# Kernel optimization log

Hardware: AMD Instinct MI355X
Metric: run time of the kernel (lower is better)

## Reference

```python
import jax, jax.numpy as jnp
import numpy as np


def setup_inputs() -> dict:
    key = jax.random.key(0)
    ks = jax.random.split(key, 4)
    B, T, D, U = 64, 2048, 256, 256
    x = jax.random.normal(ks[0], (B, T, D), dtype=jnp.float32)
    s = 1.0 / np.sqrt(D)
    kz = jax.random.normal(ks[1], (D, U), dtype=jnp.float32) * s
    kr = jax.random.normal(ks[2], (D, U), dtype=jnp.float32) * s
    kh = jax.random.normal(ks[3], (D, U), dtype=jnp.float32) * s
    return {
        'x': x, 'kz': kz, 'kr': kr, 'kh': kh,
        'mz': jnp.ones((U,), jnp.float32), 'mr': jnp.ones((U,), jnp.float32),
        'bz': jnp.zeros((U,), jnp.float32), 'br': jnp.zeros((U,), jnp.float32),
        'bh': jnp.zeros((U,), jnp.float32),
    }


def reference(x, kz, kr, kh, mz, mr, bz, br, bh):
    # Precompute the three input projections for all timesteps (batched GEMMs),
    # then scan the purely elementwise recurrence over time.
    xz = jnp.einsum('btd,du->btu', x, kz) + bz  # [B,T,U]
    xr = jnp.einsum('btd,du->btu', x, kr) + br
    xh = jnp.einsum('btd,du->btu', x, kh) + bh
    B, T, U = xz.shape
    h0 = jnp.zeros((B, U), x.dtype)

    def step(h, inp):
        xz_t, xr_t, xh_t = inp
        r = jnp.tanh(xr_t + h * mr) + 1.0
        z = jax.nn.sigmoid(xz_t + h * mz)
        hh = jnp.tanh(xh_t + r * h)
        out = (1.0 - z) * hh + z * h
        return out, out

    # scan over time axis: move T to leading axis
    xs = (jnp.swapaxes(xz, 0, 1), jnp.swapaxes(xr, 0, 1), jnp.swapaxes(xh, 0, 1))
    _, ys = jax.lax.scan(step, h0, xs)
    return jnp.swapaxes(ys, 0, 1)  # [B,T,U]
```

## Files before the change

kernel.cpp:

```cpp
#include <hip/hip_runtime.h>
#include <hip/hip_bf16.h>

#define BB 64
#define TT 2048
#define DD 256
#define UU 256
#define MM (BB*TT)
#define NN (3*UU)
#define PLANE ((size_t)BB*TT*UU)

typedef _Float16 half8 __attribute__((ext_vector_type(8)));
typedef _Float16 half4 __attribute__((ext_vector_type(4)));
typedef float floatx4 __attribute__((ext_vector_type(4)));

__device__ inline float fexp2(float x){
#if __has_builtin(__builtin_amdgcn_exp2f)
  return __builtin_amdgcn_exp2f(x);
#else
  return exp2f(x);
#endif
}
__device__ inline float frcp(float x){
#if __has_builtin(__builtin_amdgcn_rcpf)
  return __builtin_amdgcn_rcpf(x);
#else
  return 1.0f/x;
#endif
}
__device__ inline float ftanh(float a){
  const float TWO_L2E = 2.8853900817779268f;
  return 1.0f - 2.0f*frcp(fexp2(TWO_L2E*a) + 1.0f);
}
__device__ inline float fsigmoid(float a){
  const float L2E = 1.4426950408889634f;
  return frcp(1.0f + fexp2(-L2E*a));
}

__global__ __launch_bounds__(256) void prep_kernel(const float* __restrict__ kz,
                                                   const float* __restrict__ kr,
                                                   const float* __restrict__ kh,
                                                   _Float16* __restrict__ K16T){
  int o = blockIdx.x*256 + threadIdx.x;
  int n = o >> 8;
  int k = o & 255;
  int p = n >> 8;
  int u = n & 255;
  const float* w = (p==0) ? kz : ((p==1) ? kr : kh);
  K16T[o] = (_Float16)w[k*UU + u];
}

__global__ __launch_bounds__(256) void xcvt_kernel(const float* __restrict__ X,
                                                   _Float16* __restrict__ X16){
  const size_t t = (size_t)blockIdx.x*256 + threadIdx.x;
  #pragma unroll
  for (int i = 0; i < 8; i++){
    const size_t u = ((size_t)i << 20) + t;
    floatx4 v = *(const floatx4*)(X + u*4);
    half4 hv;
    #pragma unroll
    for (int q = 0; q < 4; q++) hv[q] = (_Float16)v[q];
    *(half4*)(X16 + u*4) = hv;
  }
}

#define BM 128
#define BN 128
#define BK 32

__global__ __launch_bounds__(256) void gemm_kernel(const _Float16* __restrict__ X16,
                                                   const _Float16* __restrict__ K16T,
                                                   const float* __restrict__ bz,
                                                   const float* __restrict__ br,
                                                   const float* __restrict__ bh,
                                                   _Float16* __restrict__ P){
  __shared__ __align__(16) _Float16 As[BM*BK];
  __shared__ __align__(16) _Float16 Bs[BN*BK];
  const int tid = threadIdx.x;

  const int l   = blockIdx.y*6 + blockIdx.x;
  const int xcd = l & 7;
  const int idx = l >> 3;
  const int pnl = idx / 6;
  const int by  = xcd*128 + pnl;
  const int bx  = idx - pnl*6;
  const int rowBase = by*BM;
  const int nBase   = bx*BN;

  const int wave = tid >> 6, lane = tid & 63;
  const int wm = wave & 1, wn = wave >> 1;
  const int lrow = lane & 15, lkq = lane >> 4;

  floatx4 acc[4][4] = {};

  const _Float16* aSrc0 = X16 + (size_t)(rowBase + (tid >> 2))*DD + (tid & 3)*8;
  const _Float16* aSrc1 = aSrc0 + (size_t)64*DD;
  const _Float16* bSrc0 = K16T + (size_t)(nBase + (tid >> 2))*DD + (tid & 3)*8;
  const _Float16* bSrc1 = bSrc0 + (size_t)64*DD;

  for (int k0 = 0; k0 < DD; k0 += BK) {
    __syncthreads();
    __builtin_amdgcn_global_load_lds(
        (const __attribute__((address_space(1))) void*)(aSrc0 + k0),
        (__attribute__((address_space(3))) void*)(As + tid*8), 16, 0, 0);
    __builtin_amdgcn_global_load_lds(
        (const __attribute__((address_space(1))) void*)(aSrc1 + k0),
        (__attribute__((address_space(3))) void*)(As + 2048 + tid*8), 16, 0, 0);
    __builtin_amdgcn_global_load_lds(
        (const __attribute__((address_space(1))) void*)(bSrc0 + k0),
        (__attribute__((address_space(3))) void*)(Bs + tid*8), 16, 0, 0);
    __builtin_amdgcn_global_load_lds(
        (const __attribute__((address_space(1))) void*)(bSrc1 + k0),
        (__attribute__((address_space(3))) void*)(Bs + 2048 + tid*8), 16, 0, 0);
    __syncthreads();
    half8 af[4], bf[4];
    #pragma unroll
    for (int i = 0; i < 4; i++)
      af[i] = *(const half8*)&As[(wm*64 + i*16 + lrow)*BK + lkq*8];
    #pragma unroll
    for (int j = 0; j < 4; j++)
      bf[j] = *(const half8*)&Bs[(wn*64 + j*16 + lrow)*BK + lkq*8];
    #pragma unroll
    for (int i = 0; i < 4; i++)
      #pragma unroll
      for (int j = 0; j < 4; j++)
        acc[i][j] = __builtin_amdgcn_mfma_f32_16x16x32_f16(af[i], bf[j], acc[i][j], 0, 0, 0);
  }

  const int p = bx >> 1;
  const int ub = (bx & 1) * 128;
  const float* bias = (p==0) ? bz : ((p==1) ? br : bh);
  _Float16* Pp = P + (size_t)p * PLANE;
  const int bidx = rowBase >> 11;
  const int t0 = (rowBase & 2047) + wm*64 + lkq*4;
  #pragma unroll
  for (int j = 0; j < 4; j++){
    int col = ub + wn*64 + j*16 + lrow;
    float bv = bias[col];
    _Float16* rowp = Pp + (size_t)(bidx*UU + col)*TT + t0;
    #pragma unroll
    for (int i = 0; i < 4; i++){
      half4 v;
      #pragma unroll
      for (int r = 0; r < 4; r++)
        v[r] = (_Float16)(acc[i][j][r] + bv);
      *(half4*)(rowp + i*16) = v;
    }
  }
}

#define PF 16
#define NBUF 4
__global__ __launch_bounds__(64) void scan_kernel(const _Float16* __restrict__ P,
                                                  const float* __restrict__ mz,
                                                  const float* __restrict__ mr,
                                                  float* __restrict__ out){
  const int ci = blockIdx.x*64 + threadIdx.x;
  const int b = ci >> 8;
  const int u = ci & 255;
  const half8* pz = (const half8*)(P + (size_t)ci*TT);
  const half8* pr = (const half8*)(P + PLANE + (size_t)ci*TT);
  const half8* ph = (const half8*)(P + 2*PLANE + (size_t)ci*TT);
  float* po = out + (size_t)b*(TT*UU) + u;
  const float vmz = mz[u], vmr = mr[u];
  float h = 0.0f;

  half8 qz[NBUF][2], qr[NBUF][2], qh[NBUF][2];

#define LOADC(buf, c) do { \
    qz[buf][0] = pz[(c)*2];   qz[buf][1] = pz[(c)*2+1]; \
    qr[buf][0] = pr[(c)*2];   qr[buf][1] = pr[(c)*2+1]; \
    qh[buf][0] = ph[(c)*2];   qh[buf][1] = ph[(c)*2+1]; \
  } while(0)

#define PROC(buf, c) do { \
    _Pragma("unroll") \
    for (int i = 0; i < PF; i++){ \
      float xz = (float)qz[buf][i>>3][i&7]; \
      float xr = (float)qr[buf][i>>3][i&7]; \
      float xh = (float)qh[buf][i>>3][i&7]; \
      float r  = ftanh(xr + h*vmr) + 1.0f; \
      float z  = fsigmoid(xz + h*vmz); \
      float hh = ftanh(xh + r*h); \
      h = (1.0f - z)*hh + z*h; \
      po[(size_t)((c)*PF + i)*UU] = h; \
    } \
    if ((c) + NBUF < NC) LOADC(buf, (c) + NBUF); \
  } while(0)

  const int NC = TT/PF;
  LOADC(0, 0); LOADC(1, 1); LOADC(2, 2); LOADC(3, 3);
  for (int c = 0; c < NC; c += NBUF){
    PROC(0, c);
    PROC(1, c+1);
    PROC(2, c+2);
    PROC(3, c+3);
  }
#undef LOADC
#undef PROC
}

extern "C" void kernel_launch(void* const* d_in, const int* in_sizes, int n_in,
                              void* d_out, int out_size, void* d_ws, size_t ws_size,
                              hipStream_t stream) {
  (void)in_sizes; (void)n_in; (void)out_size; (void)ws_size;
  const float* x  = (const float*)d_in[0];
  const float* kz = (const float*)d_in[1];
  const float* kr = (const float*)d_in[2];
  const float* kh = (const float*)d_in[3];
  const float* mz = (const float*)d_in[4];
  const float* mr = (const float*)d_in[5];
  const float* bz = (const float*)d_in[6];
  const float* br = (const float*)d_in[7];
  const float* bh = (const float*)d_in[8];
  float* out = (float*)d_out;

  _Float16* K16T = (_Float16*)d_ws;
  _Float16* P    = (_Float16*)((char*)d_ws + 393216);
  _Float16* X16  = (_Float16*)d_out;

  hipLaunchKernelGGL(xcvt_kernel, dim3(4096), dim3(256), 0, stream, x, X16);
  hipLaunchKernelGGL(prep_kernel, dim3(NN*DD/256), dim3(256), 0, stream, kz, kr, kh, K16T);
  hipLaunchKernelGGL(gemm_kernel, dim3(NN/BN, MM/BM), dim3(256), 0, stream,
                     X16, K16T, bz, br, bh, P);
  hipLaunchKernelGGL(scan_kernel, dim3(256), dim3(64), 0, stream, P, mz, mr, out);
}
```

Measured before the change: 474.3 us.

## Double-buffer GEMM LDS, fold activation scales into projections, interleave two scan chains

The GEMM now double-buffers its LDS tiles so the next K slice loads while the current one feeds the MFMAs, with one barrier per step instead of two. The exp2 scale factors of sigmoid and tanh are folded into the projection outputs in the GEMM epilogue and into the recurrence weights, so the scan does fewer multiplies per step. The scan gives each thread two independent hidden units, halving the grid to 128 blocks, so two dependent chains can hide each other's latency. The costs are fewer scan waves across the GPU, scaled fp16 values stored in P that may lose some precision, and a single barrier that may not be enough to order async LDS loads against reads of the other buffer.

Result: slower. 561.0 us (+18.3%).

```diff
diff --git a/kernel.cpp b/kernel.cpp
--- a/kernel.cpp
+++ b/kernel.cpp
@@ -26,14 +26,6 @@
 #else
   return 1.0f/x;
 #endif
-}
-__device__ inline float ftanh(float a){
-  const float TWO_L2E = 2.8853900817779268f;
-  return 1.0f - 2.0f*frcp(fexp2(TWO_L2E*a) + 1.0f);
-}
-__device__ inline float fsigmoid(float a){
-  const float L2E = 1.4426950408889634f;
-  return frcp(1.0f + fexp2(-L2E*a));
 }
 
 __global__ __launch_bounds__(256) void prep_kernel(const float* __restrict__ kz,
@@ -66,15 +58,14 @@
 #define BM 128
 #define BN 128
 #define BK 32
-
 __global__ __launch_bounds__(256) void gemm_kernel(const _Float16* __restrict__ X16,
                                                    const _Float16* __restrict__ K16T,
                                                    const float* __restrict__ bz,
                                                    const float* __restrict__ br,
                                                    const float* __restrict__ bh,
                                                    _Float16* __restrict__ P){
-  __shared__ __align__(16) _Float16 As[BM*BK];
-  __shared__ __align__(16) _Float16 Bs[BN*BK];
+  __shared__ __align__(16) _Float16 As[2][BM*BK];
+  __shared__ __align__(16) _Float16 Bs[2][BN*BK];
   const int tid = threadIdx.x;
 
   const int l   = blockIdx.y*6 + blockIdx.x;
@@ -97,38 +88,48 @@
   const _Float16* bSrc0 = K16T + (size_t)(nBase + (tid >> 2))*DD + (tid & 3)*8;
   const _Float16* bSrc1 = bSrc0 + (size_t)64*DD;
 
-  for (int k0 = 0; k0 < DD; k0 += BK) {
-    __syncthreads();
-    __builtin_amdgcn_global_load_lds(
-        (const __attribute__((address_space(1))) void*)(aSrc0 + k0),
-        (__attribute__((address_space(3))) void*)(As + tid*8), 16, 0, 0);
-    __builtin_amdgcn_global_load_lds(
-        (const __attribute__((address_space(1))) void*)(aSrc1 + k0),
-        (__attribute__((address_space(3))) void*)(As + 2048 + tid*8), 16, 0, 0);
-    __builtin_amdgcn_global_load_lds(
-        (const __attribute__((address_space(1))) void*)(bSrc0 + k0),
-        (__attribute__((address_space(3))) void*)(Bs + tid*8), 16, 0, 0);
-    __builtin_amdgcn_global_load_lds(
-        (const __attribute__((address_space(1))) void*)(bSrc1 + k0),
-        (__attribute__((address_space(3))) void*)(Bs + 2048 + tid*8), 16, 0, 0);
-    __syncthreads();
+#define STAGE(buf, k0) do { \
+    __builtin_amdgcn_global_load_lds( \
+        (const __attribute__((address_space(1))) void*)(aSrc0 + (k0)), \
+        (__attribute__((address_space(3))) void*)(&As[(buf)][tid*8]), 16, 0, 0); \
+    __builtin_amdgcn_global_load_lds( \
+        (const __attribute__((address_space(1))) void*)(aSrc1 + (k0)), \
+        (__attribute__((address_space(3))) void*)(&As[(buf)][2048 + tid*8]), 16, 0, 0); \
+    __builtin_amdgcn_global_load_lds( \
+        (const __attribute__((address_space(1))) void*)(bSrc0 + (k0)), \
+        (__attribute__((address_space(3))) void*)(&Bs[(buf)][tid*8]), 16, 0, 0); \
+    __builtin_amdgcn_global_load_lds( \
+        (const __attribute__((address_space(1))) void*)(bSrc1 + (k0)), \
+        (__attribute__((address_space(3))) void*)(&Bs[(buf)][2048 + tid*8]), 16, 0, 0); \
+  } while(0)
+
+  STAGE(0, 0);
+  __syncthreads();
+
+  #pragma unroll
+  for (int kk = 0; kk < 8; kk++){
+    const int cur = kk & 1;
+    if (kk < 7) STAGE(cur ^ 1, (kk + 1)*BK);
     half8 af[4], bf[4];
     #pragma unroll
     for (int i = 0; i < 4; i++)
-      af[i] = *(const half8*)&As[(wm*64 + i*16 + lrow)*BK + lkq*8];
+      af[i] = *(const half8*)&As[cur][(wm*64 + i*16 + lrow)*BK + lkq*8];
     #pragma unroll
     for (int j = 0; j < 4; j++)
-      bf[j] = *(const half8*)&Bs[(wn*64 + j*16 + lrow)*BK + lkq*8];
+      bf[j] = *(const half8*)&Bs[cur][(wn*64 + j*16 + lrow)*BK + lkq*8];
     #pragma unroll
     for (int i = 0; i < 4; i++)
       #pragma unroll
       for (int j = 0; j < 4; j++)
         acc[i][j] = __builtin_amdgcn_mfma_f32_16x16x32_f16(af[i], bf[j], acc[i][j], 0, 0, 0);
-  }
+    __syncthreads();
+  }
+#undef STAGE
 
   const int p = bx >> 1;
   const int ub = (bx & 1) * 128;
   const float* bias = (p==0) ? bz : ((p==1) ? br : bh);
+  const float pscale = (p==0) ? -1.4426950408889634f : 2.8853900817779268f;
   _Float16* Pp = P + (size_t)p * PLANE;
   const int bidx = rowBase >> 11;
   const int t0 = (rowBase & 2047) + wm*64 + lkq*4;
@@ -142,47 +143,69 @@
       half4 v;
       #pragma unroll
       for (int r = 0; r < 4; r++)
-        v[r] = (_Float16)(acc[i][j][r] + bv);
+        v[r] = (_Float16)((acc[i][j][r] + bv) * pscale);
       *(half4*)(rowp + i*16) = v;
     }
   }
 }
 
-#define PF 16
+#define PF 8
 #define NBUF 4
-__global__ __launch_bounds__(64) void scan_kernel(const _Float16* __restrict__ P,
-                                                  const float* __restrict__ mz,
-                                                  const float* __restrict__ mr,
-                                                  float* __restrict__ out){
-  const int ci = blockIdx.x*64 + threadIdx.x;
-  const int b = ci >> 8;
-  const int u = ci & 255;
-  const half8* pz = (const half8*)(P + (size_t)ci*TT);
-  const half8* pr = (const half8*)(P + PLANE + (size_t)ci*TT);
-  const half8* ph = (const half8*)(P + 2*PLANE + (size_t)ci*TT);
-  float* po = out + (size_t)b*(TT*UU) + u;
-  const float vmz = mz[u], vmr = mr[u];
-  float h = 0.0f;
+__global__ __launch_bounds__(64, 1) void scan_kernel(const _Float16* __restrict__ P,
+                                                     const float* __restrict__ mz,
+                                                     const float* __restrict__ mr,
+                                                     float* __restrict__ out){
+  const int lid = threadIdx.x;
+  const int g   = blockIdx.x;
+  const int c0  = g*128 + lid;
+  const int c1  = c0 + 64;
+  const int b   = c0 >> 8;
+  const int u0  = c0 & 255;
+  const int u1  = u0 + 64;
+  const half8* pz0 = (const half8*)(P + (size_t)c0*TT);
+  const half8* pr0 = (const half8*)(P + PLANE + (size_t)c0*TT);
+  const half8* ph0 = (const half8*)(P + 2*PLANE + (size_t)c0*TT);
+  const half8* pz1 = (const half8*)(P + (size_t)c1*TT);
+  const half8* pr1 = (const half8*)(P + PLANE + (size_t)c1*TT);
+  const half8* ph1 = (const half8*)(P + 2*PLANE + (size_t)c1*TT);
+  float* po0 = out + (size_t)b*(TT*UU) + u0;
+  float* po1 = po0 + 64;
+  const float L2E    = 1.4426950408889634f;
+  const float F4L2E  = 5.7707801635558536f;
+  const float mz0s = -L2E*mz[u0], mr0s = 2.0f*L2E*mr[u0];
+  const float mz1s = -L2E*mz[u1], mr1s = 2.0f*L2E*mr[u1];
+  float h0 = 0.0f, h1 = 0.0f;
 
   half8 qz[NBUF][2], qr[NBUF][2], qh[NBUF][2];
 
 #define LOADC(buf, c) do { \
-    qz[buf][0] = pz[(c)*2];   qz[buf][1] = pz[(c)*2+1]; \
-    qr[buf][0] = pr[(c)*2];   qr[buf][1] = pr[(c)*2+1]; \
-    qh[buf][0] = ph[(c)*2];   qh[buf][1] = ph[(c)*2+1]; \
+    qz[buf][0] = pz0[c]; qr[buf][0] = pr0[c]; qh[buf][0] = ph0[c]; \
+    qz[buf][1] = pz1[c]; qr[buf][1] = pr1[c]; qh[buf][1] = ph1[c]; \
   } while(0)
 
 #define PROC(buf, c) do { \
     _Pragma("unroll") \
     for (int i = 0; i < PF; i++){ \
-      float xz = (float)qz[buf][i>>3][i&7]; \
-      float xr = (float)qr[buf][i>>3][i&7]; \
-      float xh = (float)qh[buf][i>>3][i&7]; \
-      float r  = ftanh(xr + h*vmr) + 1.0f; \
-      float z  = fsigmoid(xz + h*vmz); \
-      float hh = ftanh(xh + r*h); \
-      h = (1.0f - z)*hh + z*h; \
-      po[(size_t)((c)*PF + i)*UU] = h; \
+      float az0 = fmaf(h0, mz0s, (float)qz[buf][0][i]); \
+      float ar0 = fmaf(h0, mr0s, (float)qr[buf][0][i]); \
+      float az1 = fmaf(h1, mz1s, (float)qz[buf][1][i]); \
+      float ar1 = fmaf(h1, mr1s, (float)qr[buf][1][i]); \
+      float z0 = frcp(1.0f + fexp2(az0)); \
+      float z1 = frcp(1.0f + fexp2(az1)); \
+      float w0 = frcp(1.0f + fexp2(ar0)); \
+      float w1 = frcp(1.0f + fexp2(ar1)); \
+      float r20 = fmaf(w0, -F4L2E, F4L2E); \
+      float r21 = fmaf(w1, -F4L2E, F4L2E); \
+      float ah0 = fmaf(r20, h0, (float)qh[buf][0][i]); \
+      float ah1 = fmaf(r21, h1, (float)qh[buf][1][i]); \
+      float v0 = frcp(1.0f + fexp2(ah0)); \
+      float v1 = frcp(1.0f + fexp2(ah1)); \
+      float hh0 = fmaf(v0, -2.0f, 1.0f); \
+      float hh1 = fmaf(v1, -2.0f, 1.0f); \
+      h0 = fmaf(z0, h0 - hh0, hh0); \
+      h1 = fmaf(z1, h1 - hh1, hh1); \
+      po0[(size_t)((c)*PF + i)*UU] = h0; \
+      po1[(size_t)((c)*PF + i)*UU] = h1; \
     } \
     if ((c) + NBUF < NC) LOADC(buf, (c) + NBUF); \
   } while(0)
@@ -222,5 +245,5 @@
   hipLaunchKernelGGL(prep_kernel, dim3(NN*DD/256), dim3(256), 0, stream, kz, kr, kh, K16T);
   hipLaunchKernelGGL(gemm_kernel, dim3(NN/BN, MM/BM), dim3(256), 0, stream,
                      X16, K16T, bz, br, bh, P);
-  hipLaunchKernelGGL(scan_kernel, dim3(256), dim3(64), 0, stream, P, mz, mr, out);
-}
+  hipLaunchKernelGGL(scan_kernel, dim3(128), dim3(64), 0, stream, P, mz, mr, out);
+}
```
